# Kernel tuning notes

Measured on AMD Instinct MI355X. Metric: run time of the kernel, lower is better.

The kernel has to match this reference:

```python
import jax, jax.numpy as jnp
import numpy as np

BS, SEQ, D_MODEL, N_HEADS = 4, 2048, 1024, 16
D_HEAD = D_MODEL // N_HEADS


def setup_inputs() -> dict:
    key = jax.random.key(0)
    ks = jax.random.split(key, 12)
    s = 1.0 / np.sqrt(D_MODEL)
    return {
        "Q": jax.random.normal(ks[0], (BS, SEQ, D_MODEL), jnp.float32),
        "K": jax.random.normal(ks[1], (BS, SEQ, D_MODEL), jnp.float32),
        "V": jax.random.normal(ks[2], (BS, SEQ, D_MODEL), jnp.float32),
        "mask": jax.random.randint(ks[3], (BS, 1, 1, SEQ), 0, 2, jnp.int32),
        "Wq": jax.random.normal(ks[4], (D_MODEL, D_MODEL), jnp.float32) * s,
        "bq": jnp.zeros((D_MODEL,), jnp.float32),
        "Wk": jax.random.normal(ks[5], (D_MODEL, D_MODEL), jnp.float32) * s,
        "bk": jnp.zeros((D_MODEL,), jnp.float32),
        "Wv": jax.random.normal(ks[6], (D_MODEL, D_MODEL), jnp.float32) * s,
        "bv": jnp.zeros((D_MODEL,), jnp.float32),
        "Wo": jax.random.normal(ks[7], (D_MODEL, D_MODEL), jnp.float32) * s,
        "bo": jnp.zeros((D_MODEL,), jnp.float32),
    }


def _split_heads(x):
    # (b, s, d_model) -> (b, h, s, d_head)
    b, s, _ = x.shape
    return x.reshape(b, s, N_HEADS, D_HEAD).transpose(0, 2, 1, 3)


def reference(Q, K, V, mask, Wq, bq, Wk, bk, Wv, bv, Wo, bo):
    q = _split_heads(Q @ Wq.T + bq)
    k = _split_heads(K @ Wk.T + bk)
    v = _split_heads(V @ Wv.T + bv)
    # (b, h, sq, sk) score matrix, scaled by sqrt(d_head)
    scores = jnp.einsum("bhqd,bhkd->bhqk", q, k) / np.sqrt(D_HEAD).astype(np.float32)
    scores = jnp.where(mask == 0, jnp.float32(-1e9), scores)
    attn = jax.nn.softmax(scores, axis=-1)
    ctx = jnp.einsum("bhqk,bhkd->bhqd", attn, v)
    b, h, s, d = ctx.shape
    ctx = ctx.transpose(0, 2, 1, 3).reshape(b, s, h * d)
    return ctx @ Wo.T + bo
```

## Files before the change

### kernel.cpp

```cpp
#include <hip/hip_runtime.h>


typedef __attribute__((ext_vector_type(8))) unsigned short us8;
typedef __attribute__((ext_vector_type(4))) unsigned short us4;
typedef __attribute__((ext_vector_type(4))) int i4;
typedef __attribute__((ext_vector_type(4))) float f4;
typedef __attribute__((ext_vector_type(4))) float f32x4;
typedef __attribute__((ext_vector_type(8))) __bf16 bf16x8;
typedef __attribute__((ext_vector_type(2))) unsigned u32x2;
typedef __attribute__((ext_vector_type(4))) unsigned u32x4;

#define DEV static __device__ __forceinline__

DEV unsigned short f2bf(float f){
  unsigned u = __builtin_bit_cast(unsigned, f);
  u = (u + 0x7fffu + ((u >> 16) & 1u)) >> 16;
  return (unsigned short)u;
}

DEV bf16x8 ld_frag(const unsigned short* p){
  return __builtin_bit_cast(bf16x8, *(const us8*)p);
}

DEV void gll16(const unsigned short* gsrc, unsigned short* ldst){
  __builtin_amdgcn_global_load_lds(
      (const __attribute__((address_space(1))) unsigned int*)gsrc,
      (__attribute__((address_space(3))) unsigned int*)ldst, 16, 0, 0);
}

DEV us8 ld_cvt_f32x8(const float* p){
  f4 v0 = *(const f4*)p;
  f4 v1 = *(const f4*)(p + 4);
  unsigned d0, d1, d2, d3;
  asm("v_cvt_pk_bf16_f32 %0, %1, %2" : "=v"(d0) : "v"(v0[0]), "v"(v0[1]));
  asm("v_cvt_pk_bf16_f32 %0, %1, %2" : "=v"(d1) : "v"(v0[2]), "v"(v0[3]));
  asm("v_cvt_pk_bf16_f32 %0, %1, %2" : "=v"(d2) : "v"(v1[0]), "v"(v1[1]));
  asm("v_cvt_pk_bf16_f32 %0, %1, %2" : "=v"(d3) : "v"(v1[2]), "v"(v1[3]));
  u32x4 u = {d0, d1, d2, d3};
  return __builtin_bit_cast(us8, u);
}

__global__ __launch_bounds__(256) void mask_scan(
    const int* __restrict__ mask, int* __restrict__ idx, int* __restrict__ nk)
{
  const int b = blockIdx.x, t = threadIdx.x;
  __shared__ int sc[256];
  int m[8]; int c = 0;
#pragma unroll
  for(int r = 0; r < 8; ++r){ m[r] = mask[b * 2048 + t * 8 + r]; c += (m[r] != 0); }
  sc[t] = c;
  __syncthreads();
  for(int s = 1; s < 256; s <<= 1){
    int v = (t >= s) ? sc[t - s] : 0;
    __syncthreads();
    sc[t] += v;
    __syncthreads();
  }
  int pos = sc[t] - c;
  int total = sc[255];
#pragma unroll
  for(int r = 0; r < 8; ++r) if(m[r]) idx[b * 2048 + pos++] = t * 8 + r;
  int pend = (total + 127) & ~127;
  for(int p = total + t; p < pend; p += 256) idx[b * 2048 + p] = 0;
  if(t == 0) nk[b] = total;
}

__global__ __launch_bounds__(256) void cvt_all(
    const float* __restrict__ Wq, const float* __restrict__ Wk,
    const float* __restrict__ Wv, const float* __restrict__ Wo,
    const float* __restrict__ Qf, const float* __restrict__ Kf, const float* __restrict__ Vf,
    unsigned short* __restrict__ Wqb, unsigned short* __restrict__ Wkb,
    unsigned short* __restrict__ Wvb, unsigned short* __restrict__ Wob,
    unsigned short* __restrict__ Qb, unsigned short* __restrict__ Kbc,
    unsigned short* __restrict__ Vbc,
    const int* __restrict__ gidx, const int* __restrict__ nkarr)
{
  const int y = blockIdx.y, x = blockIdx.x, t = threadIdx.x;
  if(y < 4){
    if(x >= 512) return;
    const float* src = (y == 0) ? Wq : (y == 1) ? Wk : (y == 2) ? Wv : Wo;
    unsigned short* dst = (y == 0) ? Wqb : (y == 1) ? Wkb : (y == 2) ? Wvb : Wob;
    size_t i = (size_t)x * 2048 + t * 8;
    *(us8*)(dst + i) = ld_cvt_f32x8(src + i);
  } else if(y == 4){
    size_t i = (size_t)x * 2048 + t * 8;
    *(us8*)(Qb + i) = ld_cvt_f32x8(Qf + i);
  } else {
    const float* src = (y == 5) ? Kf : Vf;
    unsigned short* dst = (y == 5) ? Kbc : Vbc;
    int r0 = x * 2;
    int b = r0 >> 11, j = r0 & 2047;
    if(j >= ((nkarr[b] + 127) & ~127)) return;
    int rr = t >> 7;
    int srow = gidx[b * 2048 + j + rr];
    int col = (t & 127) * 8;
    *(us8*)(dst + (size_t)(r0 + rr) * 1024 + col) =
        ld_cvt_f32x8(src + ((size_t)b * 2048 + srow) * 1024 + col);
  }
}

__global__ __launch_bounds__(256) void qkv_proj(
    const unsigned short* __restrict__ Qb, const unsigned short* __restrict__ Kbc,
    const unsigned short* __restrict__ Vbc,
    const unsigned short* __restrict__ Wqb, const unsigned short* __restrict__ Wkb,
    const unsigned short* __restrict__ Wvb,
    const float* __restrict__ bq, const float* __restrict__ bk, const float* __restrict__ bv,
    unsigned short* __restrict__ qs, unsigned short* __restrict__ ksc,
    unsigned short* __restrict__ vTc, float qscale, const int* __restrict__ nkarr)
{
  __shared__ __align__(16) unsigned short As[128 * 64];
  __shared__ __align__(16) unsigned short Bs[128 * 64];
  const int tid = threadIdx.x;
  const int x = blockIdx.x, z = blockIdx.y >> 3, ny = blockIdx.y & 7;
  const int w = tid >> 6, l = tid & 63, g = l >> 4, l15 = l & 15;
  const int wm = w >> 1, wn = w & 1;
  const int xsw = ((l & 7) ^ (l >> 3)) << 3;

  if(z >= 1){
    const int gb = (x * 128) >> 11, j0 = (x * 128) & 2047;
    if(j0 >= ((nkarr[gb] + 127) & ~127)) return;
  }

  const unsigned short* Ab = (z == 0) ? Qb : (z == 1) ? Kbc : Wvb;
  const unsigned short* Bb = (z == 0) ? Wqb : (z == 1) ? Wkb : Vbc;
  const int abase = (z == 2) ? ny * 128 : x * 128;
  const int bbase = (z == 2) ? x * 128 : ny * 128;
  const int lrow = (w << 5) + (l >> 3);

  f32x4 acc[4][4];
#pragma unroll
  for(int a = 0; a < 4; ++a)
#pragma unroll
    for(int b = 0; b < 4; ++b) acc[a][b] = (f32x4){0.f,0.f,0.f,0.f};

  for(int kt = 0; kt < 16; ++kt){
    __syncthreads();
#pragma unroll
    for(int j = 0; j < 4; ++j)
      gll16(Ab + (size_t)(abase + lrow + (j << 3)) * 1024 + kt * 64 + xsw,
            &As[((w << 5) + (j << 3)) << 6]);
#pragma unroll
    for(int j = 0; j < 4; ++j)
      gll16(Bb + (size_t)(bbase + lrow + (j << 3)) * 1024 + kt * 64 + xsw,
            &Bs[((w << 5) + (j << 3)) << 6]);
    asm volatile("s_waitcnt vmcnt(0)" ::: "memory");
    __syncthreads();
#pragma unroll
    for(int kk = 0; kk < 2; ++kk){
      bf16x8 af[4], bg[4];
#pragma unroll
      for(int mi = 0; mi < 4; ++mi){
        int row = wm * 64 + mi * 16 + l15;
        af[mi] = ld_frag(&As[row * 64 + ((kk * 32 + g * 8) ^ ((row & 7) << 3))]);
      }
#pragma unroll
      for(int ni = 0; ni < 4; ++ni){
        int row = wn * 64 + ni * 16 + l15;
        bg[ni] = ld_frag(&Bs[row * 64 + ((kk * 32 + g * 8) ^ ((row & 7) << 3))]);
      }
#pragma unroll
      for(int mi = 0; mi < 4; ++mi)
#pragma unroll
        for(int ni = 0; ni < 4; ++ni)
          acc[mi][ni] = __builtin_amdgcn_mfma_f32_16x16x32_bf16(af[mi], bg[ni], acc[mi][ni], 0, 0, 0);
    }
  }

  if(z < 2){
    const float scale = (z == 0) ? qscale : 1.0f;
    const float* bias = (z == 0) ? bq : bk;
    unsigned short* out = (z == 0) ? qs : ksc;
#pragma unroll
    for(int mi = 0; mi < 4; ++mi)
#pragma unroll
      for(int ni = 0; ni < 4; ++ni){
        int gmb = x * 128 + wm * 64 + mi * 16 + g * 4;
        int gn  = ny * 128 + wn * 64 + ni * 16 + l15;
#pragma unroll
        for(int r = 0; r < 4; ++r){
          int gm = gmb + r;
          float v = (acc[mi][ni][r] + bias[gn]) * scale;
          int b = gm >> 11, s = gm & 2047, h = gn >> 6, dh = gn & 63;
          out[(size_t)(((b << 4) + h) * 2048 + s) * 64 + dh] = f2bf(v);
        }
      }
  } else {
#pragma unroll
    for(int mi = 0; mi < 4; ++mi)
#pragma unroll
      for(int ni = 0; ni < 4; ++ni){
        int gmb = ny * 128 + wm * 64 + mi * 16 + g * 4;
        int gn  = x * 128 + wn * 64 + ni * 16 + l15;
#pragma unroll
        for(int r = 0; r < 4; ++r){
          int gm = gmb + r;
          float v = acc[mi][ni][r] + bv[gm];
          int h = gm >> 6, dh = gm & 63, b = gn >> 11, s = gn & 2047;
          vTc[(size_t)(((b << 4) + h) * 64 + dh) * 2048 + s] = f2bf(v);
        }
      }
  }
}

__global__ __launch_bounds__(256) void gemm_out(
    const unsigned short* __restrict__ Ap, const unsigned short* __restrict__ Bp,
    const float* __restrict__ bias, float* __restrict__ outp, int K)
{
  __shared__ __align__(16) unsigned short As[128 * 64];
  __shared__ __align__(16) unsigned short Bs[128 * 64];
  const int tid = threadIdx.x;
  const int gy = blockIdx.x, gx = blockIdx.y;
  const int w = tid >> 6, l = tid & 63, g = l >> 4, l15 = l & 15;
  const int wm = w >> 1, wn = w & 1;
  const int xsw = ((l & 7) ^ (l >> 3)) << 3;

  f32x4 acc[4][4];
#pragma unroll
  for(int a = 0; a < 4; ++a)
#pragma unroll
    for(int b = 0; b < 4; ++b) acc[a][b] = (f32x4){0.f,0.f,0.f,0.f};

  const int nkt = K >> 6;
  for(int kt = 0; kt < nkt; ++kt){
    __syncthreads();
#pragma unroll
    for(int j = 0; j < 4; ++j)
      gll16(Ap + (size_t)(gy * 128 + (w << 5) + (j << 3) + (l >> 3)) * K + kt * 64 + xsw,
            &As[((w << 5) + (j << 3)) << 6]);
#pragma unroll
    for(int j = 0; j < 4; ++j)
      gll16(Bp + (size_t)(gx * 128 + (w << 5) + (j << 3) + (l >> 3)) * K + kt * 64 + xsw,
            &Bs[((w << 5) + (j << 3)) << 6]);
    asm volatile("s_waitcnt vmcnt(0)" ::: "memory");
    __syncthreads();
#pragma unroll
    for(int kk = 0; kk < 2; ++kk){
      bf16x8 af[4], bg[4];
#pragma unroll
      for(int mi = 0; mi < 4; ++mi){
        int row = wm * 64 + mi * 16 + l15;
        af[mi] = ld_frag(&As[row * 64 + ((kk * 32 + g * 8) ^ ((row & 7) << 3))]);
      }
#pragma unroll
      for(int ni = 0; ni < 4; ++ni){
        int row = wn * 64 + ni * 16 + l15;
        bg[ni] = ld_frag(&Bs[row * 64 + ((kk * 32 + g * 8) ^ ((row & 7) << 3))]);
      }
#pragma unroll
      for(int mi = 0; mi < 4; ++mi)
#pragma unroll
        for(int ni = 0; ni < 4; ++ni)
          acc[mi][ni] = __builtin_amdgcn_mfma_f32_16x16x32_bf16(af[mi], bg[ni], acc[mi][ni], 0, 0, 0);
    }
  }

#pragma unroll
  for(int mi = 0; mi < 4; ++mi)
#pragma unroll
    for(int ni = 0; ni < 4; ++ni){
      int gmb = gy * 128 + wm * 64 + mi * 16 + g * 4;
      int gn  = gx * 128 + wn * 64 + ni * 16 + l15;
#pragma unroll
      for(int r = 0; r < 4; ++r)
        outp[(size_t)(gmb + r) * 1024 + gn] = acc[mi][ni][r] + bias[gn];
    }
}

__global__ __launch_bounds__(256) void attn_kernel(
    const unsigned short* __restrict__ q, const unsigned short* __restrict__ ksc,
    const unsigned short* __restrict__ vTc, const int* __restrict__ nk,
    unsigned short* __restrict__ ctx)
{
  __shared__ __align__(16) unsigned short KsB[2][64 * 64];
  __shared__ __align__(16) unsigned short VtB[2][64 * 64];
  __shared__ __align__(16) unsigned short Ps[4][16 * 64];

  const int bh = blockIdx.x;
  const int qt = blockIdx.y;
  const int b  = bh >> 4, h = bh & 15;
  const int tid = threadIdx.x;
  const int w = tid >> 6, l = tid & 63, g = l >> 4, l15 = l & 15;
  const int rl = l >> 3, c8 = l & 7;

  const int nkb = nk[b];
  const int nt = (nkb + 63) >> 6;

  const unsigned short* qbase = q + ((size_t)(bh * 2048 + qt * 64 + w * 16 + l15)) * 64;
  bf16x8 bq[2];
  bq[0] = ld_frag(qbase + g * 8);
  bq[1] = ld_frag(qbase + 32 + g * 8);

  const unsigned short* kbase = ksc + (size_t)bh * 2048 * 64;
  const unsigned short* vbase = vTc + (size_t)bh * 64 * 2048;

  const unsigned short* kg0 = kbase + (size_t)(w * 16 + rl) * 64 + c8 * 8;
  const unsigned short* vg0 = vbase + (size_t)(w * 16 + rl) * 2048 + c8 * 8;
  const int lo0 = (w * 16 + rl) * 64 + ((c8 ^ rl) << 3);
  const int lo1 = lo0 + 8 * 64;

  us8 kr0, kr1, vr0, vr1;
#define LOAD_T(kt_) do{                                        \
    kr0 = *(const us8*)(kg0 + (size_t)(kt_) * 4096);           \
    kr1 = *(const us8*)(kg0 + (size_t)(kt_) * 4096 + 512);     \
    vr0 = *(const us8*)(vg0 + (size_t)(kt_) * 64);             \
    vr1 = *(const us8*)(vg0 + (size_t)(kt_) * 64 + 8 * 2048);  \
  }while(0)
#define WRITE_T(bb_) do{                                       \
    *(us8*)&KsB[bb_][lo0] = kr0;                               \
    *(us8*)&KsB[bb_][lo1] = kr1;                               \
    *(us8*)&VtB[bb_][lo0] = vr0;                               \
    *(us8*)&VtB[bb_][lo1] = vr1;                               \
  }while(0)

  f32x4 acc[4];
#pragma unroll
  for(int mi = 0; mi < 4; ++mi) acc[mi] = (f32x4){0.f,0.f,0.f,0.f};
  float ll = 0.f;

  LOAD_T(0);
  WRITE_T(0);
  __syncthreads();

  for(int kt = 0; kt < nt; ++kt){
    const int bb = kt & 1;
    if(kt + 1 < nt) LOAD_T(kt + 1);

    f32x4 sa[4];
#pragma unroll
    for(int mi = 0; mi < 4; ++mi) sa[mi] = (f32x4){0.f,0.f,0.f,0.f};
    __builtin_amdgcn_s_setprio(1);
#pragma unroll
    for(int kk = 0; kk < 2; ++kk){
#pragma unroll
      for(int mi = 0; mi < 4; ++mi){
        int row = mi * 16 + l15;
        bf16x8 af = ld_frag(&KsB[bb][row * 64 + ((kk * 32 + g * 8) ^ ((row & 7) << 3))]);
        sa[mi] = __builtin_amdgcn_mfma_f32_16x16x32_bf16(af, bq[kk], sa[mi], 0, 0, 0);
      }
    }
    __builtin_amdgcn_s_setprio(0);

    float p[4][4];
    if((kt + 1) * 64 <= nkb){
#pragma unroll
      for(int mi = 0; mi < 4; ++mi)
#pragma unroll
        for(int r = 0; r < 4; ++r){
          p[mi][r] = __builtin_amdgcn_exp2f(sa[mi][r]);
          ll += p[mi][r];
        }
    } else {
      int kb0 = kt * 64 + g * 4;
#pragma unroll
      for(int mi = 0; mi < 4; ++mi)
#pragma unroll
        for(int r = 0; r < 4; ++r){
          float e = __builtin_amdgcn_exp2f(sa[mi][r]);
          p[mi][r] = (kb0 + mi * 16 + r < nkb) ? e : 0.f;
          ll += p[mi][r];
        }
    }

#pragma unroll
    for(int mi = 0; mi < 4; ++mi){
      unsigned d0, d1;
      asm("v_cvt_pk_bf16_f32 %0, %1, %2" : "=v"(d0) : "v"(p[mi][0]), "v"(p[mi][1]));
      asm("v_cvt_pk_bf16_f32 %0, %1, %2" : "=v"(d1) : "v"(p[mi][2]), "v"(p[mi][3]));
      u32x2 dd = {d0, d1};
      *(u32x2*)&Ps[w][l15 * 64 + ((mi * 16 + g * 4) ^ ((l15 & 7) << 3))] = dd;
    }

    __builtin_amdgcn_s_setprio(1);
#pragma unroll
    for(int kk = 0; kk < 2; ++kk){
      bf16x8 pb = ld_frag(&Ps[w][l15 * 64 + ((kk * 32 + g * 8) ^ ((l15 & 7) << 3))]);
#pragma unroll
      for(int mi = 0; mi < 4; ++mi){
        int row = mi * 16 + l15;
        bf16x8 av = ld_frag(&VtB[bb][row * 64 + ((kk * 32 + g * 8) ^ ((row & 7) << 3))]);
        acc[mi] = __builtin_amdgcn_mfma_f32_16x16x32_bf16(av, pb, acc[mi], 0, 0, 0);
      }
    }
    __builtin_amdgcn_s_setprio(0);

    if(kt + 1 < nt) WRITE_T(bb ^ 1);
    __syncthreads();
  }

  ll += __shfl_xor(ll, 16);
  ll += __shfl_xor(ll, 32);
  float inv = 1.0f / ll;

  {
    int qrow = w * 16 + l15;
#pragma unroll
    for(int mi = 0; mi < 4; ++mi){
      us4 o;
#pragma unroll
      for(int r = 0; r < 4; ++r) o[r] = f2bf(acc[mi][r] * inv);
      *(us4*)&KsB[0][qrow * 64 + ((mi * 16 + g * 4) ^ ((qrow & 7) << 3))] = o;
    }
  }
  __syncthreads();
  {
    int qrow = tid >> 2, part = tid & 3;
    us8 v0 = *(const us8*)&KsB[0][qrow * 64 + ((part * 16)     ^ ((qrow & 7) << 3))];
    us8 v1 = *(const us8*)&KsB[0][qrow * 64 + ((part * 16 + 8) ^ ((qrow & 7) << 3))];
    size_t orow = ((size_t)b * 2048 + qt * 64 + qrow) * 1024 + h * 64 + part * 16;
    *(us8*)&ctx[orow] = v0;
    *(us8*)&ctx[orow + 8] = v1;
  }
#undef LOAD_T
#undef WRITE_T
}

extern "C" void kernel_launch(void* const* d_in, const int* in_sizes, int n_in,
                              void* d_out, int out_size, void* d_ws, size_t ws_size,
                              hipStream_t stream) {
  const float* Qf = (const float*)d_in[0];
  const float* Kf = (const float*)d_in[1];
  const float* Vf = (const float*)d_in[2];
  const int*   Mk = (const int*)d_in[3];
  const float* Wq = (const float*)d_in[4];
  const float* bq = (const float*)d_in[5];
  const float* Wk = (const float*)d_in[6];
  const float* bk = (const float*)d_in[7];
  const float* Wv = (const float*)d_in[8];
  const float* bv = (const float*)d_in[9];
  const float* Wo = (const float*)d_in[10];
  const float* bo = (const float*)d_in[11];

  const size_t MB = 1u << 20;
  char* ws = (char*)d_ws;
  unsigned short* Wqb = (unsigned short*)(ws + 0 * MB);
  unsigned short* Wkb = (unsigned short*)(ws + 2 * MB);
  unsigned short* Wvb = (unsigned short*)(ws + 4 * MB);
  unsigned short* Wob = (unsigned short*)(ws + 6 * MB);
  unsigned short* qs  = (unsigned short*)(ws + 8 * MB);
  unsigned short* ksc = (unsigned short*)(ws + 24 * MB);
  unsigned short* vTc = (unsigned short*)(ws + 40 * MB);
  unsigned short* ctx = (unsigned short*)(ws + 56 * MB);
  int* idx = (int*)(ws + 72 * MB);
  int* nk  = (int*)(ws + 73 * MB);
  unsigned short* Qb  = (unsigned short*)(ws + 74 * MB);
  unsigned short* Kbc = (unsigned short*)(ws + 90 * MB);
  unsigned short* Vbc = (unsigned short*)(ws + 106 * MB);

  mask_scan<<<4, 256, 0, stream>>>(Mk, idx, nk);
  cvt_all<<<dim3(4096, 7), 256, 0, stream>>>(Wq, Wk, Wv, Wo, Qf, Kf, Vf,
                                             Wqb, Wkb, Wvb, Wob, Qb, Kbc, Vbc,
                                             idx, nk);

  const float QSCALE = 0.125f * 1.4426950408889634f;
  dim3 blk(256);
  qkv_proj<<<dim3(64, 24), blk, 0, stream>>>(Qb, Kbc, Vbc, Wqb, Wkb, Wvb,
                                             bq, bk, bv, qs, ksc, vTc, QSCALE, nk);
  attn_kernel<<<dim3(64, 32), blk, 0, stream>>>(qs, ksc, vTc, nk, ctx);
  gemm_out<<<dim3(64, 8), blk, 0, stream>>>(ctx, Wob, bo, (float*)d_out, 1024);
}
```

Baseline: 173.3 us.

## Double-buffer LDS tiles in projection GEMMs to overlap loads with MFMA

Both the QKV projection and output projection GEMMs now use two LDS buffers per operand. The next K-tile is issued via direct global-to-LDS loads before the MFMA work on the current tile, and the wait plus barrier come after the compute. This hides global memory latency behind compute and drops one barrier per iteration. In exchange LDS use doubles to 64 KB per block, which can reduce occupancy.

```diff
diff --git a/kernel.cpp b/kernel.cpp
--- a/kernel.cpp
+++ b/kernel.cpp
@@ -108,8 +108,8 @@
     unsigned short* __restrict__ qs, unsigned short* __restrict__ ksc,
     unsigned short* __restrict__ vTc, float qscale, const int* __restrict__ nkarr)
 {
-  __shared__ __align__(16) unsigned short As[128 * 64];
-  __shared__ __align__(16) unsigned short Bs[128 * 64];
+  __shared__ __align__(16) unsigned short As[2][128 * 64];
+  __shared__ __align__(16) unsigned short Bs[2][128 * 64];
   const int tid = threadIdx.x;
   const int x = blockIdx.x, z = blockIdx.y >> 3, ny = blockIdx.y & 7;
   const int w = tid >> 6, l = tid & 63, g = l >> 4, l15 = l & 15;
@@ -133,37 +133,45 @@
 #pragma unroll
     for(int b = 0; b < 4; ++b) acc[a][b] = (f32x4){0.f,0.f,0.f,0.f};
 
-  for(int kt = 0; kt < 16; ++kt){
-    __syncthreads();
+  auto STAGE = [&](int kt, int nb){
 #pragma unroll
     for(int j = 0; j < 4; ++j)
       gll16(Ab + (size_t)(abase + lrow + (j << 3)) * 1024 + kt * 64 + xsw,
-            &As[((w << 5) + (j << 3)) << 6]);
+            &As[nb][((w << 5) + (j << 3)) << 6]);
 #pragma unroll
     for(int j = 0; j < 4; ++j)
       gll16(Bb + (size_t)(bbase + lrow + (j << 3)) * 1024 + kt * 64 + xsw,
-            &Bs[((w << 5) + (j << 3)) << 6]);
+            &Bs[nb][((w << 5) + (j << 3)) << 6]);
+  };
+
+  STAGE(0, 0);
+  asm volatile("s_waitcnt vmcnt(0)" ::: "memory");
+  __syncthreads();
+
+  for(int kt = 0; kt < 16; ++kt){
+    const int cur = kt & 1, nxt = cur ^ 1;
+    if(kt + 1 < 16) STAGE(kt + 1, nxt);
+#pragma unroll
+    for(int kk = 0; kk < 2; ++kk){
+      bf16x8 af[4], bg[4];
+#pragma unroll
+      for(int mi = 0; mi < 4; ++mi){
+        int row = wm * 64 + mi * 16 + l15;
+        af[mi] = ld_frag(&As[cur][row * 64 + ((kk * 32 + g * 8) ^ ((row & 7) << 3))]);
+      }
+#pragma unroll
+      for(int ni = 0; ni < 4; ++ni){
+        int row = wn * 64 + ni * 16 + l15;
+        bg[ni] = ld_frag(&Bs[cur][row * 64 + ((kk * 32 + g * 8) ^ ((row & 7) << 3))]);
+      }
+#pragma unroll
+      for(int mi = 0; mi < 4; ++mi)
+#pragma unroll
+        for(int ni = 0; ni < 4; ++ni)
+          acc[mi][ni] = __builtin_amdgcn_mfma_f32_16x16x32_bf16(af[mi], bg[ni], acc[mi][ni], 0, 0, 0);
+    }
     asm volatile("s_waitcnt vmcnt(0)" ::: "memory");
     __syncthreads();
-#pragma unroll
-    for(int kk = 0; kk < 2; ++kk){
-      bf16x8 af[4], bg[4];
-#pragma unroll
-      for(int mi = 0; mi < 4; ++mi){
-        int row = wm * 64 + mi * 16 + l15;
-        af[mi] = ld_frag(&As[row * 64 + ((kk * 32 + g * 8) ^ ((row & 7) << 3))]);
-      }
-#pragma unroll
-      for(int ni = 0; ni < 4; ++ni){
-        int row = wn * 64 + ni * 16 + l15;
-        bg[ni] = ld_frag(&Bs[row * 64 + ((kk * 32 + g * 8) ^ ((row & 7) << 3))]);
-      }
-#pragma unroll
-      for(int mi = 0; mi < 4; ++mi)
-#pragma unroll
-        for(int ni = 0; ni < 4; ++ni)
-          acc[mi][ni] = __builtin_amdgcn_mfma_f32_16x16x32_bf16(af[mi], bg[ni], acc[mi][ni], 0, 0, 0);
-    }
   }
 
   if(z < 2){
@@ -206,13 +214,14 @@
     const unsigned short* __restrict__ Ap, const unsigned short* __restrict__ Bp,
     const float* __restrict__ bias, float* __restrict__ outp, int K)
 {
-  __shared__ __align__(16) unsigned short As[128 * 64];
-  __shared__ __align__(16) unsigned short Bs[128 * 64];
+  __shared__ __align__(16) unsigned short As[2][128 * 64];
+  __shared__ __align__(16) unsigned short Bs[2][128 * 64];
   const int tid = threadIdx.x;
   const int gy = blockIdx.x, gx = blockIdx.y;
   const int w = tid >> 6, l = tid & 63, g = l >> 4, l15 = l & 15;
   const int wm = w >> 1, wn = w & 1;
   const int xsw = ((l & 7) ^ (l >> 3)) << 3;
+  const int lrow = (w << 5) + (l >> 3);
 
   f32x4 acc[4][4];
 #pragma unroll
@@ -220,38 +229,46 @@
 #pragma unroll
     for(int b = 0; b < 4; ++b) acc[a][b] = (f32x4){0.f,0.f,0.f,0.f};
 
+  auto STAGE = [&](int kt, int nb){
+#pragma unroll
+    for(int j = 0; j < 4; ++j)
+      gll16(Ap + (size_t)(gy * 128 + lrow + (j << 3)) * K + kt * 64 + xsw,
+            &As[nb][((w << 5) + (j << 3)) << 6]);
+#pragma unroll
+    for(int j = 0; j < 4; ++j)
+      gll16(Bp + (size_t)(gx * 128 + lrow + (j << 3)) * K + kt * 64 + xsw,
+            &Bs[nb][((w << 5) + (j << 3)) << 6]);
+  };
+
   const int nkt = K >> 6;
+  STAGE(0, 0);
+  asm volatile("s_waitcnt vmcnt(0)" ::: "memory");
+  __syncthreads();
+
   for(int kt = 0; kt < nkt; ++kt){
-    __syncthreads();
-#pragma unroll
-    for(int j = 0; j < 4; ++j)
-      gll16(Ap + (size_t)(gy * 128 + (w << 5) + (j << 3) + (l >> 3)) * K + kt * 64 + xsw,
-            &As[((w << 5) + (j << 3)) << 6]);
-#pragma unroll
-    for(int j = 0; j < 4; ++j)
-      gll16(Bp + (size_t)(gx * 128 + (w << 5) + (j << 3) + (l >> 3)) * K + kt * 64 + xsw,
-            &Bs[((w << 5) + (j << 3)) << 6]);
+    const int cur = kt & 1, nxt = cur ^ 1;
+    if(kt + 1 < nkt) STAGE(kt + 1, nxt);
+#pragma unroll
+    for(int kk = 0; kk < 2; ++kk){
+      bf16x8 af[4], bg[4];
+#pragma unroll
+      for(int mi = 0; mi < 4; ++mi){
+        int row = wm * 64 + mi * 16 + l15;
+        af[mi] = ld_frag(&As[cur][row * 64 + ((kk * 32 + g * 8) ^ ((row & 7) << 3))]);
+      }
+#pragma unroll
+      for(int ni = 0; ni < 4; ++ni){
+        int row = wn * 64 + ni * 16 + l15;
+        bg[ni] = ld_frag(&Bs[cur][row * 64 + ((kk * 32 + g * 8) ^ ((row & 7) << 3))]);
+      }
+#pragma unroll
+      for(int mi = 0; mi < 4; ++mi)
+#pragma unroll
+        for(int ni = 0; ni < 4; ++ni)
+          acc[mi][ni] = __builtin_amdgcn_mfma_f32_16x16x32_bf16(af[mi], bg[ni], acc[mi][ni], 0, 0, 0);
+    }
     asm volatile("s_waitcnt vmcnt(0)" ::: "memory");
     __syncthreads();
-#pragma unroll
-    for(int kk = 0; kk < 2; ++kk){
-      bf16x8 af[4], bg[4];
-#pragma unroll
-      for(int mi = 0; mi < 4; ++mi){
-        int row = wm * 64 + mi * 16 + l15;
-        af[mi] = ld_frag(&As[row * 64 + ((kk * 32 + g * 8) ^ ((row & 7) << 3))]);
-      }
-#pragma unroll
-      for(int ni = 0; ni < 4; ++ni){
-        int row = wn * 64 + ni * 16 + l15;
-        bg[ni] = ld_frag(&Bs[row * 64 + ((kk * 32 + g * 8) ^ ((row & 7) << 3))]);
-      }
-#pragma unroll
-      for(int mi = 0; mi < 4; ++mi)
-#pragma unroll
-        for(int ni = 0; ni < 4; ++ni)
-          acc[mi][ni] = __builtin_amdgcn_mfma_f32_16x16x32_bf16(af[mi], bg[ni], acc[mi][ni], 0, 0, 0);
-    }
   }
 
 #pragma unroll
```

Result: no change. 173.3 us (+0.0%).

## Process two 64-row query tiles per attention block to reuse K/V tiles

Applied to the files above, without the earlier changes.

Each attention workgroup now handles 128 query rows (two 64-row sub-tiles) instead of 64, so every K/V tile loaded into shared memory serves twice as many queries. The goal is to halve global K/V traffic and the load/sync overhead per query. The grid shrinks from 2048 to 1024 blocks, and register and LDS use per block go up, which can lower occupancy and parallelism. The masked and full softmax branches are also merged into one predicated path.

```diff
diff --git a/kernel.cpp b/kernel.cpp
--- a/kernel.cpp
+++ b/kernel.cpp
@@ -273,7 +273,8 @@
 {
   __shared__ __align__(16) unsigned short KsB[2][64 * 64];
   __shared__ __align__(16) unsigned short VtB[2][64 * 64];
-  __shared__ __align__(16) unsigned short Ps[4][16 * 64];
+  __shared__ __align__(16) unsigned short Ps0[4][16 * 64];
+  __shared__ __align__(16) unsigned short Ps1[4][16 * 64];
 
   const int bh = blockIdx.x;
   const int qt = blockIdx.y;
@@ -285,10 +286,13 @@
   const int nkb = nk[b];
   const int nt = (nkb + 63) >> 6;
 
-  const unsigned short* qbase = q + ((size_t)(bh * 2048 + qt * 64 + w * 16 + l15)) * 64;
-  bf16x8 bq[2];
-  bq[0] = ld_frag(qbase + g * 8);
-  bq[1] = ld_frag(qbase + 32 + g * 8);
+  const unsigned short* qbase0 = q + ((size_t)(bh * 2048 + qt * 128 + w * 16 + l15)) * 64;
+  const unsigned short* qbase1 = qbase0 + 64 * 64;
+  bf16x8 bq0[2], bq1[2];
+  bq0[0] = ld_frag(qbase0 + g * 8);
+  bq0[1] = ld_frag(qbase0 + 32 + g * 8);
+  bq1[0] = ld_frag(qbase1 + g * 8);
+  bq1[1] = ld_frag(qbase1 + 32 + g * 8);
 
   const unsigned short* kbase = ksc + (size_t)bh * 2048 * 64;
   const unsigned short* vbase = vTc + (size_t)bh * 64 * 2048;
@@ -312,10 +316,13 @@
     *(us8*)&VtB[bb_][lo1] = vr1;                               \
   }while(0)
 
-  f32x4 acc[4];
-#pragma unroll
-  for(int mi = 0; mi < 4; ++mi) acc[mi] = (f32x4){0.f,0.f,0.f,0.f};
-  float ll = 0.f;
+  f32x4 acc0[4], acc1[4];
+#pragma unroll
+  for(int mi = 0; mi < 4; ++mi){
+    acc0[mi] = (f32x4){0.f,0.f,0.f,0.f};
+    acc1[mi] = (f32x4){0.f,0.f,0.f,0.f};
+  }
+  float ll0 = 0.f, ll1 = 0.f;
 
   LOAD_T(0);
   WRITE_T(0);
@@ -325,90 +332,143 @@
     const int bb = kt & 1;
     if(kt + 1 < nt) LOAD_T(kt + 1);
 
-    f32x4 sa[4];
-#pragma unroll
-    for(int mi = 0; mi < 4; ++mi) sa[mi] = (f32x4){0.f,0.f,0.f,0.f};
-    __builtin_amdgcn_s_setprio(1);
-#pragma unroll
-    for(int kk = 0; kk < 2; ++kk){
-#pragma unroll
-      for(int mi = 0; mi < 4; ++mi){
-        int row = mi * 16 + l15;
-        bf16x8 af = ld_frag(&KsB[bb][row * 64 + ((kk * 32 + g * 8) ^ ((row & 7) << 3))]);
-        sa[mi] = __builtin_amdgcn_mfma_f32_16x16x32_bf16(af, bq[kk], sa[mi], 0, 0, 0);
-      }
-    }
-    __builtin_amdgcn_s_setprio(0);
-
-    float p[4][4];
-    if((kt + 1) * 64 <= nkb){
-#pragma unroll
-      for(int mi = 0; mi < 4; ++mi)
-#pragma unroll
-        for(int r = 0; r < 4; ++r){
-          p[mi][r] = __builtin_amdgcn_exp2f(sa[mi][r]);
-          ll += p[mi][r];
-        }
-    } else {
-      int kb0 = kt * 64 + g * 4;
+    const bool full = (kt + 1) * 64 <= nkb;
+    const int kb0 = kt * 64 + g * 4;
+
+    {
+      f32x4 sa[4];
+#pragma unroll
+      for(int mi = 0; mi < 4; ++mi) sa[mi] = (f32x4){0.f,0.f,0.f,0.f};
+      __builtin_amdgcn_s_setprio(1);
+#pragma unroll
+      for(int kk = 0; kk < 2; ++kk)
+#pragma unroll
+        for(int mi = 0; mi < 4; ++mi){
+          int row = mi * 16 + l15;
+          bf16x8 af = ld_frag(&KsB[bb][row * 64 + ((kk * 32 + g * 8) ^ ((row & 7) << 3))]);
+          sa[mi] = __builtin_amdgcn_mfma_f32_16x16x32_bf16(af, bq0[kk], sa[mi], 0, 0, 0);
+        }
+      __builtin_amdgcn_s_setprio(0);
+
+      float p[4][4];
 #pragma unroll
       for(int mi = 0; mi < 4; ++mi)
 #pragma unroll
         for(int r = 0; r < 4; ++r){
           float e = __builtin_amdgcn_exp2f(sa[mi][r]);
-          p[mi][r] = (kb0 + mi * 16 + r < nkb) ? e : 0.f;
-          ll += p[mi][r];
-        }
+          p[mi][r] = (full || (kb0 + mi * 16 + r < nkb)) ? e : 0.f;
+          ll0 += p[mi][r];
+        }
+
+#pragma unroll
+      for(int mi = 0; mi < 4; ++mi){
+        unsigned d0, d1;
+        asm("v_cvt_pk_bf16_f32 %0, %1, %2" : "=v"(d0) : "v"(p[mi][0]), "v"(p[mi][1]));
+        asm("v_cvt_pk_bf16_f32 %0, %1, %2" : "=v"(d1) : "v"(p[mi][2]), "v"(p[mi][3]));
+        u32x2 dd = {d0, d1};
+        *(u32x2*)&Ps0[w][l15 * 64 + ((mi * 16 + g * 4) ^ ((l15 & 7) << 3))] = dd;
+      }
+
+      __builtin_amdgcn_s_setprio(1);
+#pragma unroll
+      for(int kk = 0; kk < 2; ++kk){
+        bf16x8 pb = ld_frag(&Ps0[w][l15 * 64 + ((kk * 32 + g * 8) ^ ((l15 & 7) << 3))]);
+#pragma unroll
+        for(int mi = 0; mi < 4; ++mi){
+          int row = mi * 16 + l15;
+          bf16x8 av = ld_frag(&VtB[bb][row * 64 + ((kk * 32 + g * 8) ^ ((row & 7) << 3))]);
+          acc0[mi] = __builtin_amdgcn_mfma_f32_16x16x32_bf16(av, pb, acc0[mi], 0, 0, 0);
+        }
+      }
+      __builtin_amdgcn_s_setprio(0);
     }
 
-#pragma unroll
-    for(int mi = 0; mi < 4; ++mi){
-      unsigned d0, d1;
-      asm("v_cvt_pk_bf16_f32 %0, %1, %2" : "=v"(d0) : "v"(p[mi][0]), "v"(p[mi][1]));
-      asm("v_cvt_pk_bf16_f32 %0, %1, %2" : "=v"(d1) : "v"(p[mi][2]), "v"(p[mi][3]));
-      u32x2 dd = {d0, d1};
-      *(u32x2*)&Ps[w][l15 * 64 + ((mi * 16 + g * 4) ^ ((l15 & 7) << 3))] = dd;
+    {
+      f32x4 sa[4];
+#pragma unroll
+      for(int mi = 0; mi < 4; ++mi) sa[mi] = (f32x4){0.f,0.f,0.f,0.f};
+      __builtin_amdgcn_s_setprio(1);
+#pragma unroll
+      for(int kk = 0; kk < 2; ++kk)
+#pragma unroll
+        for(int mi = 0; mi < 4; ++mi){
+          int row = mi * 16 + l15;
+          bf16x8 af = ld_frag(&KsB[bb][row * 64 + ((kk * 32 + g * 8) ^ ((row & 7) << 3))]);
+          sa[mi] = __builtin_amdgcn_mfma_f32_16x16x32_bf16(af, bq1[kk], sa[mi], 0, 0, 0);
+        }
+      __builtin_amdgcn_s_setprio(0);
+
+      float p[4][4];
+#pragma unroll
+      for(int mi = 0; mi < 4; ++mi)
+#pragma unroll
+        for(int r = 0; r < 4; ++r){
+          float e = __builtin_amdgcn_exp2f(sa[mi][r]);
+          p[mi][r] = (full || (kb0 + mi * 16 + r < nkb)) ? e : 0.f;
+          ll1 += p[mi][r];
+        }
+
+#pragma unroll
+      for(int mi = 0; mi < 4; ++mi){
+        unsigned d0, d1;
+        asm("v_cvt_pk_bf16_f32 %0, %1, %2" : "=v"(d0) : "v"(p[mi][0]), "v"(p[mi][1]));
+        asm("v_cvt_pk_bf16_f32 %0, %1, %2" : "=v"(d1) : "v"(p[mi][2]), "v"(p[mi][3]));
+        u32x2 dd = {d0, d1};
+        *(u32x2*)&Ps1[w][l15 * 64 + ((mi * 16 + g * 4) ^ ((l15 & 7) << 3))] = dd;
+      }
+
+      __builtin_amdgcn_s_setprio(1);
+#pragma unroll
+      for(int kk = 0; kk < 2; ++kk){
+        bf16x8 pb = ld_frag(&Ps1[w][l15 * 64 + ((kk * 32 + g * 8) ^ ((l15 & 7) << 3))]);
+#pragma unroll
+        for(int mi = 0; mi < 4; ++mi){
+          int row = mi * 16 + l15;
+          bf16x8 av = ld_frag(&VtB[bb][row * 64 + ((kk * 32 + g * 8) ^ ((row & 7) << 3))]);
+          acc1[mi] = __builtin_amdgcn_mfma_f32_16x16x32_bf16(av, pb, acc1[mi], 0, 0, 0);
+        }
+      }
+      __builtin_amdgcn_s_setprio(0);
     }
 
-    __builtin_amdgcn_s_setprio(1);
-#pragma unroll
-    for(int kk = 0; kk < 2; ++kk){
-      bf16x8 pb = ld_frag(&Ps[w][l15 * 64 + ((kk * 32 + g * 8) ^ ((l15 & 7) << 3))]);
-#pragma unroll
-      for(int mi = 0; mi < 4; ++mi){
-        int row = mi * 16 + l15;
-        bf16x8 av = ld_frag(&VtB[bb][row * 64 + ((kk * 32 + g * 8) ^ ((row & 7) << 3))]);
-        acc[mi] = __builtin_amdgcn_mfma_f32_16x16x32_bf16(av, pb, acc[mi], 0, 0, 0);
-      }
-    }
-    __builtin_amdgcn_s_setprio(0);
-
     if(kt + 1 < nt) WRITE_T(bb ^ 1);
     __syncthreads();
   }
 
-  ll += __shfl_xor(ll, 16);
-  ll += __shfl_xor(ll, 32);
-  float inv = 1.0f / ll;
+  ll0 += __shfl_xor(ll0, 16); ll0 += __shfl_xor(ll0, 32);
+  ll1 += __shfl_xor(ll1, 16); ll1 += __shfl_xor(ll1, 32);
+  float inv0 = 1.0f / ll0, inv1 = 1.0f / ll1;
 
   {
     int qrow = w * 16 + l15;
 #pragma unroll
     for(int mi = 0; mi < 4; ++mi){
-      us4 o;
-#pragma unroll
-      for(int r = 0; r < 4; ++r) o[r] = f2bf(acc[mi][r] * inv);
-      *(us4*)&KsB[0][qrow * 64 + ((mi * 16 + g * 4) ^ ((qrow & 7) << 3))] = o;
+      us4 o0, o1;
+#pragma unroll
+      for(int r = 0; r < 4; ++r){
+        o0[r] = f2bf(acc0[mi][r] * inv0);
+        o1[r] = f2bf(acc1[mi][r] * inv1);
+      }
+      int off = qrow * 64 + ((mi * 16 + g * 4) ^ ((qrow & 7) << 3));
+      *(us4*)&KsB[0][off] = o0;
+      *(us4*)&VtB[0][off] = o1;
     }
   }
   __syncthreads();
   {
     int qrow = tid >> 2, part = tid & 3;
-    us8 v0 = *(const us8*)&KsB[0][qrow * 64 + ((part * 16)     ^ ((qrow & 7) << 3))];
-    us8 v1 = *(const us8*)&KsB[0][qrow * 64 + ((part * 16 + 8) ^ ((qrow & 7) << 3))];
-    size_t orow = ((size_t)b * 2048 + qt * 64 + qrow) * 1024 + h * 64 + part * 16;
-    *(us8*)&ctx[orow] = v0;
-    *(us8*)&ctx[orow + 8] = v1;
+    int off0 = qrow * 64 + ((part * 16)     ^ ((qrow & 7) << 3));
+    int off1 = qrow * 64 + ((part * 16 + 8) ^ ((qrow & 7) << 3));
+    us8 a0 = *(const us8*)&KsB[0][off0];
+    us8 a1 = *(const us8*)&KsB[0][off1];
+    us8 b0 = *(const us8*)&VtB[0][off0];
+    us8 b1 = *(const us8*)&VtB[0][off1];
+    size_t orow0 = ((size_t)b * 2048 + qt * 128 + qrow) * 1024 + h * 64 + part * 16;
+    size_t orow1 = orow0 + (size_t)64 * 1024;
+    *(us8*)&ctx[orow0] = a0;
+    *(us8*)&ctx[orow0 + 8] = a1;
+    *(us8*)&ctx[orow1] = b0;
+    *(us8*)&ctx[orow1 + 8] = b1;
   }
 #undef LOAD_T
 #undef WRITE_T
@@ -455,6 +515,6 @@
   dim3 blk(256);
   qkv_proj<<<dim3(64, 24), blk, 0, stream>>>(Qb, Kbc, Vbc, Wqb, Wkb, Wvb,
                                              bq, bk, bv, qs, ksc, vTc, QSCALE, nk);
-  attn_kernel<<<dim3(64, 32), blk, 0, stream>>>(qs, ksc, vTc, nk, ctx);
+  attn_kernel<<<dim3(64, 16), blk, 0, stream>>>(qs, ksc, vTc, nk, ctx);
   gemm_out<<<dim3(64, 8), blk, 0, stream>>>(ctx, Wob, bo, (float*)d_out, 1024);
 }
```

Result: slower. 182.6 us (+5.4%).
